# Kernel optimization log

Hardware: AMD Instinct MI355X
Metric: run time of the kernel (lower is better)

Reference implementation:

```python
import jax, jax.numpy as jnp
import numpy as np

B, T, D = 2, 2048, 2048
N_HEADS, N_KV, HEAD_DIM = 16, 8, 128
SOFTCAP = 50.0
BIG_NEG = -2.3819763e38
ROPE_BASE = 10000.0


def apply_rope(x, positions):
    # x: [B, L, N, H], positions: [B, L]
    H = x.shape[-1]
    half = H // 2
    fraction = 2.0 * jnp.arange(half, dtype=jnp.float32) / H
    timescale = ROPE_BASE ** fraction  # [H/2]
    sinusoid = positions.astype(jnp.float32)[:, :, None, None] / timescale[None, None, None, :]  # [B,L,1,H/2]
    sin, cos = jnp.sin(sinusoid), jnp.cos(sinusoid)
    first, second = jnp.split(x, 2, axis=-1)
    out = jnp.concatenate([first * cos - second * sin, second * cos + first * sin], axis=-1)
    return out.astype(x.dtype)


def setup_inputs() -> dict:
    key = jax.random.key(0)
    k1, k2, k3, k4 = jax.random.split(key, 4)
    x = jax.random.normal(k1, (B, T, D), dtype=jnp.float32)
    positions = jnp.broadcast_to(jnp.arange(T, dtype=jnp.int32), (B, T))
    # causal mask [B, 1, T, S]
    attn_mask = jnp.broadcast_to(jnp.tril(jnp.ones((T, T), dtype=bool))[None, None], (B, 1, T, T))
    s = 1.0 / np.sqrt(D)
    w_q = jax.random.normal(k2, (N_HEADS, D, HEAD_DIM), dtype=jnp.float32) * s
    w_kv = jax.random.normal(k3, (2, N_KV, D, HEAD_DIM), dtype=jnp.float32) * s
    w_out = jax.random.normal(k4, (N_HEADS, HEAD_DIM, D), dtype=jnp.float32) * (1.0 / np.sqrt(N_HEADS * HEAD_DIM))
    return {"x": x, "positions": positions, "attn_mask": attn_mask, "w_q": w_q, "w_kv": w_kv, "w_out": w_out}


def reference(x, positions, attn_mask, w_q, w_kv, w_out):
    # projections (GQA branch: num_kv_heads != num_heads)
    q = jnp.einsum('btd,ndh->btnh', x, w_q)            # [B,T,N,H]
    kv = jnp.einsum('bsd,cndh->cbsnh', x, w_kv)        # [2,B,S,K,H]
    k, v = kv[0], kv[1]
    q = apply_rope(q, positions) * (HEAD_DIM ** -0.5)  # rsqrt_head_dim
    k = apply_rope(k, positions)
    G = N_HEADS // N_KV
    q = q.reshape(B, T, N_KV, G, HEAD_DIM)             # B T K G H
    logits = jnp.einsum('btkgh,bskh->bkgts', q, k).astype(jnp.float32)
    logits = jnp.tanh(logits / SOFTCAP) * SOFTCAP
    masked = jnp.where(attn_mask[:, :, None, :, :], logits, BIG_NEG)
    probs = jax.nn.softmax(masked, axis=-1).astype(k.dtype)
    encoded = jnp.einsum('bkgts,bskh->btkgh', probs, v).reshape(B, T, N_HEADS, HEAD_DIM)
    return jnp.einsum('btnh,nhd->btd', encoded, w_out)
```

## Files before the change

### kernel.cpp

```cpp
#include <hip/hip_runtime.h>


typedef unsigned short u16;
typedef __attribute__((ext_vector_type(8))) short short8;
typedef __attribute__((ext_vector_type(4))) float floatx4;

static __device__ __forceinline__ u16 f2b(float f){
  unsigned u = __float_as_uint(f);
  u = (u + 0x7fffu + ((u >> 16) & 1u)) >> 16;
  return (u16)u;
}
static __device__ __forceinline__ float b2f(u16 u){
  return __uint_as_float(((unsigned)u) << 16);
}
static __device__ __forceinline__ void gload16(const u16* g, u16* l){
  __builtin_amdgcn_global_load_lds(
      (const __attribute__((address_space(1))) unsigned int*)g,
      (__attribute__((address_space(3))) unsigned int*)l, 16, 0, 0);
}

static __device__ void tr64(const float* __restrict__ s, u16* __restrict__ d,
                            int sRS, int dRS, float (*t)[65], int tid){
  #pragma unroll
  for(int i = 0; i < 16; i++){
    int idx = tid + 256 * i;
    t[idx >> 6][idx & 63] = s[(long)(idx >> 6) * sRS + (idx & 63)];
  }
  __syncthreads();
  #pragma unroll
  for(int i = 0; i < 16; i++){
    int idx = tid + 256 * i;
    d[(long)(idx >> 6) * dRS + (idx & 63)] = f2b(t[idx & 63][idx >> 6]);
  }
}

__global__ __launch_bounds__(256) void k_prep(
    const float* __restrict__ x, u16* __restrict__ xb,
    const float* __restrict__ wq, u16* __restrict__ wq_t,
    const float* __restrict__ wkv, u16* __restrict__ wkv_t,
    const float* __restrict__ wo, u16* __restrict__ wo_t,
    const int* __restrict__ pos, float* __restrict__ tab){
  __shared__ float t[64][65];
  int blk = blockIdx.x, tid = threadIdx.x;
  if(blk < 8192){
    int i = blk * 256 + tid;
    float4 v = ((const float4*)x)[i];
    ushort4 o = make_ushort4(f2b(v.x), f2b(v.y), f2b(v.z), f2b(v.w));
    ((ushort4*)xb)[i] = o;
  } else if(blk < 9216){
    int q = blk - 8192;
    int bx = q & 1, by = (q >> 1) & 31, bz = q >> 6;
    tr64(wq + (long)bz * 262144 + (long)by * 64 * 128 + bx * 64,
         wq_t + (long)bz * 262144 + (long)bx * 64 * 2048 + by * 64, 128, 2048, t, tid);
  } else if(blk < 10240){
    int q = blk - 9216;
    int bx = q & 1, by = (q >> 1) & 31, bz = q >> 6;
    tr64(wkv + (long)bz * 262144 + (long)by * 64 * 128 + bx * 64,
         wkv_t + (long)bz * 262144 + (long)bx * 64 * 2048 + by * 64, 128, 2048, t, tid);
  } else if(blk < 11264){
    int q = blk - 10240;
    int bx = q & 31, by = q >> 5;
    tr64(wo + (long)by * 64 * 2048 + bx * 64,
         wo_t + (long)bx * 64 * 2048 + by * 64, 2048, 2048, t, tid);
  } else {
    int idx = (blk - 11264) * 256 + tid;
    int row = idx >> 6, h = idx & 63;
    float pf = (float)pos[row];
    float inv = exp2f(-0.20762050593045077f * (float)h);
    float ang = pf * inv;
    tab[(row << 7) + h]      = sinf(ang);
    tab[(row << 7) + 64 + h] = cosf(ang);
  }
}

#define STAGE_A(tt, h) do{ \
  const u16* s_ = Ag + (tt) * 64 + (h) * 262144; \
  u16* d_ = ld + ss * 8192; \
  gload16(s_, d_); gload16(s_ + 131072, d_ + 4096); \
  ss++; if(ss == 10) ss = 0; }while(0)
#define STAGE_B(tt, h) do{ \
  const u16* s_ = Bg + (tt) * 64 + (h) * 262144; \
  u16* d_ = ld + ss * 8192; \
  gload16(s_, d_); gload16(s_ + 131072, d_ + 4096); \
  ss++; if(ss == 10) ss = 0; }while(0)

__global__ __launch_bounds__(512, 2) void k_gemm_qkv(
    const u16* __restrict__ A, const u16* __restrict__ wq_t, const u16* __restrict__ wkv_t,
    const float* __restrict__ tab,
    u16* __restrict__ qb, u16* __restrict__ kb, u16* __restrict__ vtp){
  __shared__ __attribute__((aligned(16))) u16 ring[81920];
  int lin = blockIdx.x + (blockIdx.y << 4);
  int xcd = lin & 7, jj = lin >> 3;
  int mt = (xcd & 3) * 4 + (jj & 3);
  int nt = (xcd >> 2) * 8 + (jj >> 2);
  const u16* Bt = (nt < 8) ? (wq_t + (long)nt * 524288)
                           : (wkv_t + (long)(nt - 8) * 524288);
  int tid = threadIdx.x;
  int lane = tid & 63, wave = tid >> 6, l15 = lane & 15, quad = lane >> 4;
  int wr = wave >> 2, wc = wave & 3;
  int cq0 = quad ^ (l15 & 7), cq1 = cq0 ^ 4;
  int srow = tid >> 3;
  int gch  = (tid & 7) ^ (srow & 7);
  const u16* Ag = A  + ((long)mt * 256 + srow) * 2048 + (gch << 3);
  const u16* Bg = Bt + (long)srow * 2048 + (gch << 3);
  u16* ld = ring + tid * 8;
  int aB = l15 << 6;
  int bB = ((wc & 1) * 64 + l15) << 6;
  int sa = wr;
  int sb = 2 + (wc >> 1);
  int ss = 0;
  floatx4 acc[8][4];
  const floatx4 fz = {0.f, 0.f, 0.f, 0.f};
  #pragma unroll
  for(int m = 0; m < 8; m++)
    #pragma unroll
    for(int n = 0; n < 4; n++) acc[m][n] = fz;

  STAGE_A(0, 0); STAGE_A(0, 1); STAGE_B(0, 0); STAGE_B(0, 1);
  STAGE_A(1, 0); STAGE_A(1, 1);
  asm volatile("s_waitcnt vmcnt(4)" ::: "memory");
  __builtin_amdgcn_s_barrier();

  #pragma unroll 1
  for(int t = 0; t < 32; t++){
    const u16* aS = ring + sa * 8192;
    const u16* bS = ring + sb * 8192;
    int tB = (t < 31) ? t + 1 : 31;
    int tA = (t < 30) ? t + 2 : 31;
    short8 am0k0[4], am0k1[4], am1k0[4], am1k1[4], b0[2], b1[2];
    #pragma unroll
    for(int n = 0; n < 2; n++){
      b0[n] = *(const short8*)(bS + bB + (n << 10) + (cq0 << 3));
      b1[n] = *(const short8*)(bS + bB + (n << 10) + (cq1 << 3));
    }
    #pragma unroll
    for(int m = 0; m < 4; m++){
      am0k0[m] = *(const short8*)(aS + aB + (m << 10) + (cq0 << 3));
      am0k1[m] = *(const short8*)(aS + aB + (m << 10) + (cq1 << 3));
    }
    STAGE_B(tB, 0); STAGE_B(tB, 1);
    __builtin_amdgcn_s_setprio(1);
    #pragma unroll
    for(int m = 0; m < 4; m++)
      #pragma unroll
      for(int n = 0; n < 2; n++)
        acc[m][n] = __builtin_amdgcn_mfma_f32_16x16x32_bf16(am0k0[m], b0[n], acc[m][n], 0, 0, 0);
    #pragma unroll
    for(int m = 0; m < 4; m++)
      #pragma unroll
      for(int n = 0; n < 2; n++)
        acc[m][n] = __builtin_amdgcn_mfma_f32_16x16x32_bf16(am0k1[m], b1[n], acc[m][n], 0, 0, 0);
    __builtin_amdgcn_s_setprio(0);
    #pragma unroll
    for(int m = 0; m < 4; m++){
      am1k0[m] = *(const short8*)(aS + aB + 4096 + (m << 10) + (cq0 << 3));
      am1k1[m] = *(const short8*)(aS + aB + 4096 + (m << 10) + (cq1 << 3));
    }
    STAGE_A(tA, 0);
    __builtin_amdgcn_s_setprio(1);
    #pragma unroll
    for(int m = 0; m < 4; m++)
      #pragma unroll
      for(int n = 0; n < 2; n++)
        acc[4 + m][n] = __builtin_amdgcn_mfma_f32_16x16x32_bf16(am1k0[m], b0[n], acc[4 + m][n], 0, 0, 0);
    #pragma unroll
    for(int m = 0; m < 4; m++)
      #pragma unroll
      for(int n = 0; n < 2; n++)
        acc[4 + m][n] = __builtin_amdgcn_mfma_f32_16x16x32_bf16(am1k1[m], b1[n], acc[4 + m][n], 0, 0, 0);
    __builtin_amdgcn_s_setprio(0);
    #pragma unroll
    for(int n = 0; n < 2; n++){
      b0[n] = *(const short8*)(bS + bB + ((2 + n) << 10) + (cq0 << 3));
      b1[n] = *(const short8*)(bS + bB + ((2 + n) << 10) + (cq1 << 3));
    }
    STAGE_A(tA, 1);
    __builtin_amdgcn_s_setprio(1);
    #pragma unroll
    for(int m = 0; m < 4; m++)
      #pragma unroll
      for(int n = 0; n < 2; n++)
        acc[4 + m][2 + n] = __builtin_amdgcn_mfma_f32_16x16x32_bf16(am1k0[m], b0[n], acc[4 + m][2 + n], 0, 0, 0);
    #pragma unroll
    for(int m = 0; m < 4; m++)
      #pragma unroll
      for(int n = 0; n < 2; n++)
        acc[4 + m][2 + n] = __builtin_amdgcn_mfma_f32_16x16x32_bf16(am1k1[m], b1[n], acc[4 + m][2 + n], 0, 0, 0);
    #pragma unroll
    for(int m = 0; m < 4; m++)
      #pragma unroll
      for(int n = 0; n < 2; n++)
        acc[m][2 + n] = __builtin_amdgcn_mfma_f32_16x16x32_bf16(am0k0[m], b0[n], acc[m][2 + n], 0, 0, 0);
    #pragma unroll
    for(int m = 0; m < 4; m++)
      #pragma unroll
      for(int n = 0; n < 2; n++)
        acc[m][2 + n] = __builtin_amdgcn_mfma_f32_16x16x32_bf16(am0k1[m], b1[n], acc[m][2 + n], 0, 0, 0);
    __builtin_amdgcn_s_setprio(0);
    asm volatile("s_waitcnt vmcnt(4)" ::: "memory");
    __builtin_amdgcn_s_barrier();
    sa += 4; if(sa >= 10) sa -= 10;
    sb += 4; if(sb >= 10) sb -= 10;
  }

  asm volatile("s_waitcnt vmcnt(0)" ::: "memory");
  __syncthreads();
  u16* sT = ring;
  int grow0 = mt * 256;
  int hb = wc >> 1, wcl = wc & 1;
  #pragma unroll 1
  for(int hh = 0; hh < 2; hh++){
    if(hb == hh){
      #pragma unroll
      for(int m = 0; m < 8; m++){
        int row = wr * 128 + m * 16 + quad * 4;
        #pragma unroll
        for(int n = 0; n < 4; n++){
          int colh = wcl * 64 + n * 16 + l15;
          #pragma unroll
          for(int j = 0; j < 4; j++)
            sT[(row + j) * 132 + colh] = f2b(acc[m][n][j]);
        }
      }
    }
    __syncthreads();
    if(nt < 12){
      float scale = (nt < 8) ? 0.08838834764831845f : 1.0f;
      u16* dst = (nt < 8) ? qb : kb;
      int dS   = (nt < 8) ? 2048 : 1024;
      int dcol = (nt < 8) ? (nt * 2 + hh) * 128 : ((nt - 8) * 2 + hh) * 128;
      #pragma unroll
      for(int it = 0; it < 16; it++){
        int idx = tid + 512 * it;
        int row = idx >> 5, cw = idx & 31;
        int grow = grow0 + row;
        unsigned lo = *(const unsigned*)&sT[row * 132 + 2 * cw];
        unsigned hi = *(const unsigned*)&sT[row * 132 + 64 + 2 * cw];
        float2 sn = *(const float2*)&tab[(grow << 7) + 2 * cw];
        float2 cs = *(const float2*)&tab[(grow << 7) + 64 + 2 * cw];
        float x1a = b2f((u16)lo), x1b = b2f((u16)(lo >> 16));
        float x2a = b2f((u16)hi), x2b = b2f((u16)(hi >> 16));
        float o1a = (x1a * cs.x - x2a * sn.x) * scale;
        float o1b = (x1b * cs.y - x2b * sn.y) * scale;
        float o2a = (x2a * cs.x + x1a * sn.x) * scale;
        float o2b = (x2b * cs.y + x1b * sn.y) * scale;
        unsigned w1 = (unsigned)f2b(o1a) | ((unsigned)f2b(o1b) << 16);
        unsigned w2 = (unsigned)f2b(o2a) | ((unsigned)f2b(o2b) << 16);
        *(unsigned*)&dst[(long)grow * dS + dcol + 2 * cw] = w1;
        *(unsigned*)&dst[(long)grow * dS + dcol + 64 + 2 * cw] = w2;
      }
    } else {
      int b = mt >> 3, kvh = (nt - 12) * 2 + hh;
      u16* vt = vtp + (long)(b * 8 + kvh) * 262144;
      int tcol0 = (mt & 7) * 256;
      int h = tid >> 2, s0 = (tid & 3) * 64;
      #pragma unroll
      for(int i = 0; i < 16; i++){
        int s = s0 + i * 4;
        ushort4 v4 = make_ushort4(sT[(s    ) * 132 + h], sT[(s + 1) * 132 + h],
                                  sT[(s + 2) * 132 + h], sT[(s + 3) * 132 + h]);
        *(ushort4*)&vt[(long)h * 2048 + tcol0 + s] = v4;
      }
    }
    __syncthreads();
  }
}
#undef STAGE_A
#undef STAGE_B

__global__ __launch_bounds__(256) void k_gemm_out(
    const u16* __restrict__ A, const u16* __restrict__ Bt0, float* __restrict__ C){
  __shared__ __attribute__((aligned(16))) u16 sA[128 * 64];
  __shared__ __attribute__((aligned(16))) u16 sB[128 * 64];
  int mt = blockIdx.x, nt = blockIdx.y;
  const u16* Bt = Bt0 + (long)nt * 262144;
  int tid = threadIdx.x;
  int lane = tid & 63, wave = tid >> 6, l15 = lane & 15, quad = lane >> 4;
  int ro = (wave & 1) * 64, co = (wave >> 1) * 64;
  int xm7 = l15 & 7;
  int srow = tid >> 3;
  int gch  = (tid & 7) ^ (srow & 7);
  const u16* Ag = A  + ((long)(mt * 128) + srow) * 2048 + (gch << 3);
  const u16* Bg = Bt + (long)srow * 2048 + (gch << 3);
  u16* lA = sA + tid * 8;
  u16* lB = sB + tid * 8;
  floatx4 acc[4][4];
  const floatx4 fz = {0.f, 0.f, 0.f, 0.f};
  #pragma unroll
  for(int r = 0; r < 4; r++)
    #pragma unroll
    for(int c = 0; c < 4; c++) acc[r][c] = fz;
  for(int k0 = 0; k0 < 2048; k0 += 64){
    #pragma unroll
    for(int r = 0; r < 4; r++){
      gload16(Ag + (long)r * 65536 + k0, lA + r * 2048);
      gload16(Bg + (long)r * 65536 + k0, lB + r * 2048);
    }
    __syncthreads();
    #pragma unroll
    for(int ks = 0; ks < 2; ks++){
      short8 af[4], bfr[4];
      #pragma unroll
      for(int r = 0; r < 4; r++)
        af[r]  = *(const short8*)(sA + ((ro + r * 16 + l15) << 6) + ((((ks << 2) | quad) ^ xm7) << 3));
      #pragma unroll
      for(int c = 0; c < 4; c++)
        bfr[c] = *(const short8*)(sB + ((co + c * 16 + l15) << 6) + ((((ks << 2) | quad) ^ xm7) << 3));
      #pragma unroll
      for(int r = 0; r < 4; r++)
        #pragma unroll
        for(int c = 0; c < 4; c++)
          acc[r][c] = __builtin_amdgcn_mfma_f32_16x16x32_bf16(af[r], bfr[c], acc[r][c], 0, 0, 0);
    }
    __syncthreads();
  }
  long rb0 = (long)mt * 128 + ro + quad * 4;
  #pragma unroll
  for(int r = 0; r < 4; r++)
    #pragma unroll
    for(int c = 0; c < 4; c++){
      int col = nt * 128 + co + c * 16 + l15;
      #pragma unroll
      for(int j = 0; j < 4; j++)
        C[(rb0 + r * 16 + j) * 2048 + col] = acc[r][c][j];
    }
}

__global__ __launch_bounds__(256) void k_flash(
    const u16* __restrict__ qb, const u16* __restrict__ kb,
    const u16* __restrict__ vt, u16* __restrict__ enc){
  __shared__ __attribute__((aligned(16))) u16 sK[2 * 64 * 128];
  __shared__ __attribute__((aligned(16))) u16 sVt[2 * 128 * 64];
  __shared__ __attribute__((aligned(16))) u16 sP[4][16][72];
  int qt = 31 - blockIdx.y;
  int hidx = blockIdx.x;
  int b = hidx >> 4, kv = (hidx >> 1) & 7, g = hidx & 1;
  int tid = threadIdx.x;
  int lane = tid & 63, wave = tid >> 6, l15 = lane & 15, quad = lane >> 4;

  short8 qf[4];
  {
    const u16* qg = qb + ((long)b * 2048 + qt * 64 + wave * 16 + l15) * 2048
                       + (kv * 2 + g) * 128 + quad * 8;
    #pragma unroll
    for(int ks = 0; ks < 4; ks++) qf[ks] = *(const short8*)(qg + ks * 32);
  }

  int krow = tid >> 4;
  int kch  = (tid & 15) ^ krow;
  const u16* Kg = kb + ((long)b * 2048 + krow) * 1024 + kv * 128 + (kch << 3);
  int vrow = tid >> 3;
  int vch  = (tid & 7) ^ (vrow & 7);
  const u16* Vg = vt + ((long)(b * 8 + kv) * 128 + vrow) * 2048 + (vch << 3);
  u16* lK = sK  + tid * 8;
  u16* lV = sVt + tid * 8;
  #pragma unroll
  for(int r = 0; r < 4; r++){
    gload16(Kg + (long)r * 16384, lK + r * 2048);
    gload16(Vg + (long)r * 65536, lV + r * 2048);
  }

  float l_loc[4] = {0.f, 0.f, 0.f, 0.f};
  floatx4 o_acc[8];
  const floatx4 fz = {0.f, 0.f, 0.f, 0.f};
  #pragma unroll
  for(int c = 0; c < 8; c++) o_acc[c] = fz;

  const float c1 = 0.057707801635558536f;
  const float c2 = -144.26950408889634f;
  const float c3 = 72.13475204444817f;

  for(int kt = 0; kt <= qt; kt++){
    int buf = (kt & 1) * 8192;
    __syncthreads();
    if(kt < qt){
      int nb = buf ^ 8192;
      #pragma unroll
      for(int r = 0; r < 4; r++){
        gload16(Kg + (long)(kt + 1) * 65536 + (long)r * 16384, lK + nb + r * 2048);
        gload16(Vg + (kt + 1) * 64 + (long)r * 65536, lV + nb + r * 2048);
      }
    }
    floatx4 s_acc[4];
    #pragma unroll
    for(int c = 0; c < 4; c++) s_acc[c] = fz;
    #pragma unroll
    for(int ks = 0; ks < 4; ks++){
      #pragma unroll
      for(int cb = 0; cb < 4; cb++){
        short8 bk = *(const short8*)(sK + buf + ((cb * 16 + l15) << 7)
                                     + ((((ks << 2) | quad) ^ l15) << 3));
        s_acc[cb] = __builtin_amdgcn_mfma_f32_16x16x32_bf16(qf[ks], bk, s_acc[cb], 0, 0, 0);
      }
    }
    if(kt < qt){
      #pragma unroll
      for(int r = 0; r < 4; r++){
        #pragma unroll
        for(int cb = 0; cb < 4; cb++){
          float s = s_acc[cb][r];
          float u = __builtin_amdgcn_exp2f(c1 * s);
          float d = __builtin_amdgcn_rcpf(u + 1.f);
          float p = __builtin_amdgcn_exp2f(__builtin_fmaf(c2, d, c3));
          l_loc[r] += p;
          sP[wave][quad * 4 + r][cb * 16 + l15] = f2b(p);
        }
      }
    } else {
      int rloc = wave * 16 + quad * 4;
      #pragma unroll
      for(int r = 0; r < 4; r++){
        #pragma unroll
        for(int cb = 0; cb < 4; cb++){
          float s = s_acc[cb][r];
          float u = __builtin_amdgcn_exp2f(c1 * s);
          float d = __builtin_amdgcn_rcpf(u + 1.f);
          float p = __builtin_amdgcn_exp2f(__builtin_fmaf(c2, d, c3));
          if(cb * 16 + l15 > rloc + r) p = 0.f;
          l_loc[r] += p;
          sP[wave][quad * 4 + r][cb * 16 + l15] = f2b(p);
        }
      }
    }
    #pragma unroll
    for(int ks2 = 0; ks2 < 2; ks2++){
      short8 ap = *(const short8*)&sP[wave][l15][ks2 * 32 + quad * 8];
      #pragma unroll
      for(int c = 0; c < 8; c++){
        short8 bv = *(const short8*)(sVt + buf + ((c * 16 + l15) << 6)
                                     + ((((ks2 << 2) | quad) ^ (l15 & 7)) << 3));
        o_acc[c] = __builtin_amdgcn_mfma_f32_16x16x32_bf16(ap, bv, o_acc[c], 0, 0, 0);
      }
    }
  }
  #pragma unroll
  for(int r = 0; r < 4; r++){
    float l = l_loc[r];
    #pragma unroll
    for(int off = 1; off < 16; off <<= 1) l += __shfl_xor(l, off);
    float invl = 1.f / l;
    long rowe = (long)b * 2048 + qt * 64 + wave * 16 + quad * 4 + r;
    #pragma unroll
    for(int c = 0; c < 8; c++)
      enc[rowe * 2048 + (kv * 2 + g) * 128 + c * 16 + l15] = f2b(o_acc[c][r] * invl);
  }
}

extern "C" void kernel_launch(void* const* d_in, const int* in_sizes, int n_in,
                              void* d_out, int out_size, void* d_ws, size_t ws_size,
                              hipStream_t stream){
  const float* x     = (const float*)d_in[0];
  const int*   posi  = (const int*)  d_in[1];
  const float* w_q   = (const float*)d_in[3];
  const float* w_kv  = (const float*)d_in[4];
  const float* w_out = (const float*)d_in[5];
  float* out = (float*)d_out;

  char* w = (char*)d_ws;
  u16* xb     = (u16*)(w);
  u16* wq_t   = (u16*)(w + 16777216);
  u16* wkv_t  = (u16*)(w + 25165824);
  u16* wout_t = (u16*)(w + 33554432);
  u16* q_buf  = (u16*)(w + 41943040);
  u16* k_buf  = (u16*)(w + 58720256);
  u16* v_t    = (u16*)(w + 67108864);
  float* tab  = (float*)(w + 75497472);
  u16* enc    = xb;

  k_prep    <<<12288, 256, 0, stream>>>(x, xb, w_q, wq_t, w_kv, wkv_t, w_out, wout_t, posi, tab);
  k_gemm_qkv<<<dim3(16, 16), 512, 0, stream>>>(xb, wq_t, wkv_t, tab, q_buf, k_buf, v_t);
  k_flash   <<<dim3(32, 32), 256, 0, stream>>>(q_buf, k_buf, v_t, enc);
  k_gemm_out<<<dim3(32, 16), 256, 0, stream>>>(enc, wout_t, out);
}
```

Measured before the change: 311.9 us.

## Double flash query tile to 128 rows with 8 waves sharing K/V loads

The flash kernel now processes 128 query rows per block with 512 threads (8 waves) instead of 64 rows with 256 threads, so each K/V tile loaded into shared memory is reused by twice as many waves. The pipeline is restructured: K is double-buffered while V uses a single buffer loaded per iteration, with explicit vmcnt waits and raw barriers splitting the QK and PV phases. Waves whose rows lie entirely before the current key tile skip work. This halves global K/V traffic but adds more barriers per iteration, and causal imbalance across waves within a block may leave some waves idle.

Measured after the change: 318.1 us. No clear change (+2.0%).

```diff
diff --git a/kernel.cpp b/kernel.cpp
--- a/kernel.cpp
+++ b/kernel.cpp
@@ -326,13 +326,13 @@
     }
 }
 
-__global__ __launch_bounds__(256) void k_flash(
+__global__ __launch_bounds__(512, 4) void k_flash(
     const u16* __restrict__ qb, const u16* __restrict__ kb,
     const u16* __restrict__ vt, u16* __restrict__ enc){
   __shared__ __attribute__((aligned(16))) u16 sK[2 * 64 * 128];
-  __shared__ __attribute__((aligned(16))) u16 sVt[2 * 128 * 64];
-  __shared__ __attribute__((aligned(16))) u16 sP[4][16][72];
-  int qt = 31 - blockIdx.y;
+  __shared__ __attribute__((aligned(16))) u16 sV[128 * 64];
+  __shared__ __attribute__((aligned(16))) u16 sP[8][16][72];
+  int qt = 15 - blockIdx.y;
   int hidx = blockIdx.x;
   int b = hidx >> 4, kv = (hidx >> 1) & 7, g = hidx & 1;
   int tid = threadIdx.x;
@@ -340,25 +340,23 @@
 
   short8 qf[4];
   {
-    const u16* qg = qb + ((long)b * 2048 + qt * 64 + wave * 16 + l15) * 2048
+    const u16* qg = qb + ((long)b * 2048 + qt * 128 + wave * 16 + l15) * 2048
                        + (kv * 2 + g) * 128 + quad * 8;
     #pragma unroll
     for(int ks = 0; ks < 4; ks++) qf[ks] = *(const short8*)(qg + ks * 32);
   }
 
   int krow = tid >> 4;
-  int kch  = (tid & 15) ^ krow;
+  int kch  = (tid & 15) ^ (krow & 15);
   const u16* Kg = kb + ((long)b * 2048 + krow) * 1024 + kv * 128 + (kch << 3);
   int vrow = tid >> 3;
   int vch  = (tid & 7) ^ (vrow & 7);
   const u16* Vg = vt + ((long)(b * 8 + kv) * 128 + vrow) * 2048 + (vch << 3);
-  u16* lK = sK  + tid * 8;
-  u16* lV = sVt + tid * 8;
-  #pragma unroll
-  for(int r = 0; r < 4; r++){
-    gload16(Kg + (long)r * 16384, lK + r * 2048);
-    gload16(Vg + (long)r * 65536, lV + r * 2048);
-  }
+  u16* lK = sK + tid * 8;
+  u16* lV = sV + tid * 8;
+
+  int KT = 2 * qt + 2;
+  gload16(Kg, lK); gload16(Kg + 32768, lK + 4096);
 
   float l_loc[4] = {0.f, 0.f, 0.f, 0.f};
   floatx4 o_acc[8];
@@ -370,68 +368,76 @@
   const float c2 = -144.26950408889634f;
   const float c3 = 72.13475204444817f;
 
-  for(int kt = 0; kt <= qt; kt++){
+  #pragma unroll 1
+  for(int kt = 0; kt < KT; kt++){
     int buf = (kt & 1) * 8192;
-    __syncthreads();
-    if(kt < qt){
-      int nb = buf ^ 8192;
-      #pragma unroll
-      for(int r = 0; r < 4; r++){
-        gload16(Kg + (long)(kt + 1) * 65536 + (long)r * 16384, lK + nb + r * 2048);
-        gload16(Vg + (kt + 1) * 64 + (long)r * 65536, lV + nb + r * 2048);
-      }
-    }
-    floatx4 s_acc[4];
-    #pragma unroll
-    for(int c = 0; c < 4; c++) s_acc[c] = fz;
-    #pragma unroll
-    for(int ks = 0; ks < 4; ks++){
-      #pragma unroll
-      for(int cb = 0; cb < 4; cb++){
-        short8 bk = *(const short8*)(sK + buf + ((cb * 16 + l15) << 7)
-                                     + ((((ks << 2) | quad) ^ l15) << 3));
-        s_acc[cb] = __builtin_amdgcn_mfma_f32_16x16x32_bf16(qf[ks], bk, s_acc[cb], 0, 0, 0);
-      }
-    }
-    if(kt < qt){
-      #pragma unroll
-      for(int r = 0; r < 4; r++){
+    int tn = (kt + 1 < KT) ? kt + 1 : KT - 1;
+    gload16(Vg + kt * 64, lV);
+    gload16(Vg + kt * 64 + 131072, lV + 4096);
+    gload16(Kg + (long)tn * 65536, lK + (buf ^ 8192));
+    gload16(Kg + (long)tn * 65536 + 32768, lK + (buf ^ 8192) + 4096);
+    asm volatile("s_waitcnt vmcnt(4)" ::: "memory");
+    __builtin_amdgcn_s_barrier();
+    int rrel = qt * 128 + wave * 16 - kt * 64;
+    bool act = (rrel + 15 >= 0);
+    if(act){
+      floatx4 s_acc[4];
+      #pragma unroll
+      for(int c = 0; c < 4; c++) s_acc[c] = fz;
+      #pragma unroll
+      for(int ks = 0; ks < 4; ks++){
         #pragma unroll
         for(int cb = 0; cb < 4; cb++){
-          float s = s_acc[cb][r];
-          float u = __builtin_amdgcn_exp2f(c1 * s);
-          float d = __builtin_amdgcn_rcpf(u + 1.f);
-          float p = __builtin_amdgcn_exp2f(__builtin_fmaf(c2, d, c3));
-          l_loc[r] += p;
-          sP[wave][quad * 4 + r][cb * 16 + l15] = f2b(p);
+          short8 bk = *(const short8*)(sK + buf + ((cb * 16 + l15) << 7)
+                                       + ((((ks << 2) | quad) ^ l15) << 3));
+          s_acc[cb] = __builtin_amdgcn_mfma_f32_16x16x32_bf16(qf[ks], bk, s_acc[cb], 0, 0, 0);
         }
       }
-    } else {
-      int rloc = wave * 16 + quad * 4;
-      #pragma unroll
-      for(int r = 0; r < 4; r++){
-        #pragma unroll
-        for(int cb = 0; cb < 4; cb++){
-          float s = s_acc[cb][r];
-          float u = __builtin_amdgcn_exp2f(c1 * s);
-          float d = __builtin_amdgcn_rcpf(u + 1.f);
-          float p = __builtin_amdgcn_exp2f(__builtin_fmaf(c2, d, c3));
-          if(cb * 16 + l15 > rloc + r) p = 0.f;
-          l_loc[r] += p;
-          sP[wave][quad * 4 + r][cb * 16 + l15] = f2b(p);
+      if(rrel >= 63){
+        #pragma unroll
+        for(int r = 0; r < 4; r++){
+          #pragma unroll
+          for(int cb = 0; cb < 4; cb++){
+            float s = s_acc[cb][r];
+            float u = __builtin_amdgcn_exp2f(c1 * s);
+            float d = __builtin_amdgcn_rcpf(u + 1.f);
+            float p = __builtin_amdgcn_exp2f(__builtin_fmaf(c2, d, c3));
+            l_loc[r] += p;
+            sP[wave][quad * 4 + r][cb * 16 + l15] = f2b(p);
+          }
         }
-      }
-    }
-    #pragma unroll
-    for(int ks2 = 0; ks2 < 2; ks2++){
-      short8 ap = *(const short8*)&sP[wave][l15][ks2 * 32 + quad * 8];
-      #pragma unroll
-      for(int c = 0; c < 8; c++){
-        short8 bv = *(const short8*)(sVt + buf + ((c * 16 + l15) << 6)
-                                     + ((((ks2 << 2) | quad) ^ (l15 & 7)) << 3));
-        o_acc[c] = __builtin_amdgcn_mfma_f32_16x16x32_bf16(ap, bv, o_acc[c], 0, 0, 0);
-      }
-    }
+      } else {
+        int dbase = rrel + quad * 4;
+        #pragma unroll
+        for(int r = 0; r < 4; r++){
+          #pragma unroll
+          for(int cb = 0; cb < 4; cb++){
+            float s = s_acc[cb][r];
+            float u = __builtin_amdgcn_exp2f(c1 * s);
+            float d = __builtin_amdgcn_rcpf(u + 1.f);
+            float p = __builtin_amdgcn_exp2f(__builtin_fmaf(c2, d, c3));
+            if(cb * 16 + l15 > dbase + r) p = 0.f;
+            l_loc[r] += p;
+            sP[wave][quad * 4 + r][cb * 16 + l15] = f2b(p);
+          }
+        }
+      }
+    }
+    asm volatile("s_waitcnt vmcnt(2)" ::: "memory");
+    __builtin_amdgcn_s_barrier();
+    if(act){
+      #pragma unroll
+      for(int ks2 = 0; ks2 < 2; ks2++){
+        short8 ap = *(const short8*)&sP[wave][l15][ks2 * 32 + quad * 8];
+        #pragma unroll
+        for(int c = 0; c < 8; c++){
+          short8 bv = *(const short8*)(sV + ((c * 16 + l15) << 6)
+                                       + ((((ks2 << 2) | quad) ^ (l15 & 7)) << 3));
+          o_acc[c] = __builtin_amdgcn_mfma_f32_16x16x32_bf16(ap, bv, o_acc[c], 0, 0, 0);
+        }
+      }
+    }
+    __builtin_amdgcn_s_barrier();
   }
   #pragma unroll
   for(int r = 0; r < 4; r++){
@@ -439,7 +445,7 @@
     #pragma unroll
     for(int off = 1; off < 16; off <<= 1) l += __shfl_xor(l, off);
     float invl = 1.f / l;
-    long rowe = (long)b * 2048 + qt * 64 + wave * 16 + quad * 4 + r;
+    long rowe = (long)b * 2048 + qt * 128 + wave * 16 + quad * 4 + r;
     #pragma unroll
     for(int c = 0; c < 8; c++)
       enc[rowe * 2048 + (kv * 2 + g) * 128 + c * 16 + l15] = f2b(o_acc[c][r] * invl);
@@ -469,6 +475,6 @@
 
   k_prep    <<<12288, 256, 0, stream>>>(x, xb, w_q, wq_t, w_kv, wkv_t, w_out, wout_t, posi, tab);
   k_gemm_qkv<<<dim3(16, 16), 512, 0, stream>>>(xb, wq_t, wkv_t, tab, q_buf, k_buf, v_t);
-  k_flash   <<<dim3(32, 32), 256, 0, stream>>>(q_buf, k_buf, v_t, enc);
+  k_flash   <<<dim3(32, 16), 512, 0, stream>>>(q_buf, k_buf, v_t, enc);
   k_gemm_out<<<dim3(32, 16), 256, 0, stream>>>(enc, wout_t, out);
 }
```

## Process both GQA query heads per block to share K/V tile loads

Applied to the files above, without the earlier changes.

Each flash-attention block now handles both query heads of a KV group, so every K and V tile staged in LDS is used by two sets of MFMAs. This halves the grid and the global K/V traffic. The q-tile order is also changed to mix long and short causal rows. The cost is doubled accumulator registers (two o_acc sets and two score sets), which may lower occupancy, and half as many blocks to spread across CUs.

Result: slower. 356.1 us (+14.2%).

```diff
diff --git a/kernel.cpp b/kernel.cpp
--- a/kernel.cpp
+++ b/kernel.cpp
@@ -332,18 +332,22 @@
   __shared__ __attribute__((aligned(16))) u16 sK[2 * 64 * 128];
   __shared__ __attribute__((aligned(16))) u16 sVt[2 * 128 * 64];
   __shared__ __attribute__((aligned(16))) u16 sP[4][16][72];
-  int qt = 31 - blockIdx.y;
+  int by = blockIdx.y;
+  int qt = (by < 16) ? (31 - by) : (by - 16);
   int hidx = blockIdx.x;
-  int b = hidx >> 4, kv = (hidx >> 1) & 7, g = hidx & 1;
+  int b = hidx >> 3, kv = hidx & 7;
   int tid = threadIdx.x;
   int lane = tid & 63, wave = tid >> 6, l15 = lane & 15, quad = lane >> 4;
 
-  short8 qf[4];
+  short8 qf0[4], qf1[4];
   {
     const u16* qg = qb + ((long)b * 2048 + qt * 64 + wave * 16 + l15) * 2048
-                       + (kv * 2 + g) * 128 + quad * 8;
-    #pragma unroll
-    for(int ks = 0; ks < 4; ks++) qf[ks] = *(const short8*)(qg + ks * 32);
+                       + kv * 256 + quad * 8;
+    #pragma unroll
+    for(int ks = 0; ks < 4; ks++){
+      qf0[ks] = *(const short8*)(qg + ks * 32);
+      qf1[ks] = *(const short8*)(qg + 128 + ks * 32);
+    }
   }
 
   int krow = tid >> 4;
@@ -360,11 +364,12 @@
     gload16(Vg + (long)r * 65536, lV + r * 2048);
   }
 
-  float l_loc[4] = {0.f, 0.f, 0.f, 0.f};
-  floatx4 o_acc[8];
+  float l0[4] = {0.f, 0.f, 0.f, 0.f};
+  float l1[4] = {0.f, 0.f, 0.f, 0.f};
+  floatx4 o0[8], o1[8];
   const floatx4 fz = {0.f, 0.f, 0.f, 0.f};
   #pragma unroll
-  for(int c = 0; c < 8; c++) o_acc[c] = fz;
+  for(int c = 0; c < 8; c++){ o0[c] = fz; o1[c] = fz; }
 
   const float c1 = 0.057707801635558536f;
   const float c2 = -144.26950408889634f;
@@ -381,45 +386,32 @@
         gload16(Vg + (kt + 1) * 64 + (long)r * 65536, lV + nb + r * 2048);
       }
     }
-    floatx4 s_acc[4];
-    #pragma unroll
-    for(int c = 0; c < 4; c++) s_acc[c] = fz;
+    floatx4 s0[4], s1[4];
+    #pragma unroll
+    for(int c = 0; c < 4; c++){ s0[c] = fz; s1[c] = fz; }
     #pragma unroll
     for(int ks = 0; ks < 4; ks++){
       #pragma unroll
       for(int cb = 0; cb < 4; cb++){
         short8 bk = *(const short8*)(sK + buf + ((cb * 16 + l15) << 7)
                                      + ((((ks << 2) | quad) ^ l15) << 3));
-        s_acc[cb] = __builtin_amdgcn_mfma_f32_16x16x32_bf16(qf[ks], bk, s_acc[cb], 0, 0, 0);
-      }
-    }
-    if(kt < qt){
-      #pragma unroll
-      for(int r = 0; r < 4; r++){
-        #pragma unroll
-        for(int cb = 0; cb < 4; cb++){
-          float s = s_acc[cb][r];
-          float u = __builtin_amdgcn_exp2f(c1 * s);
-          float d = __builtin_amdgcn_rcpf(u + 1.f);
-          float p = __builtin_amdgcn_exp2f(__builtin_fmaf(c2, d, c3));
-          l_loc[r] += p;
-          sP[wave][quad * 4 + r][cb * 16 + l15] = f2b(p);
-        }
-      }
-    } else {
-      int rloc = wave * 16 + quad * 4;
-      #pragma unroll
-      for(int r = 0; r < 4; r++){
-        #pragma unroll
-        for(int cb = 0; cb < 4; cb++){
-          float s = s_acc[cb][r];
-          float u = __builtin_amdgcn_exp2f(c1 * s);
-          float d = __builtin_amdgcn_rcpf(u + 1.f);
-          float p = __builtin_amdgcn_exp2f(__builtin_fmaf(c2, d, c3));
-          if(cb * 16 + l15 > rloc + r) p = 0.f;
-          l_loc[r] += p;
-          sP[wave][quad * 4 + r][cb * 16 + l15] = f2b(p);
-        }
+        s0[cb] = __builtin_amdgcn_mfma_f32_16x16x32_bf16(qf0[ks], bk, s0[cb], 0, 0, 0);
+        s1[cb] = __builtin_amdgcn_mfma_f32_16x16x32_bf16(qf1[ks], bk, s1[cb], 0, 0, 0);
+      }
+    }
+    int rloc = wave * 16 + quad * 4;
+    bool diag = (kt == qt);
+    #pragma unroll
+    for(int r = 0; r < 4; r++){
+      #pragma unroll
+      for(int cb = 0; cb < 4; cb++){
+        float s = s0[cb][r];
+        float u = __builtin_amdgcn_exp2f(c1 * s);
+        float d = __builtin_amdgcn_rcpf(u + 1.f);
+        float p = __builtin_amdgcn_exp2f(__builtin_fmaf(c2, d, c3));
+        if(diag && (cb * 16 + l15 > rloc + r)) p = 0.f;
+        l0[r] += p;
+        sP[wave][quad * 4 + r][cb * 16 + l15] = f2b(p);
       }
     }
     #pragma unroll
@@ -429,20 +421,48 @@
       for(int c = 0; c < 8; c++){
         short8 bv = *(const short8*)(sVt + buf + ((c * 16 + l15) << 6)
                                      + ((((ks2 << 2) | quad) ^ (l15 & 7)) << 3));
-        o_acc[c] = __builtin_amdgcn_mfma_f32_16x16x32_bf16(ap, bv, o_acc[c], 0, 0, 0);
+        o0[c] = __builtin_amdgcn_mfma_f32_16x16x32_bf16(ap, bv, o0[c], 0, 0, 0);
+      }
+    }
+    #pragma unroll
+    for(int r = 0; r < 4; r++){
+      #pragma unroll
+      for(int cb = 0; cb < 4; cb++){
+        float s = s1[cb][r];
+        float u = __builtin_amdgcn_exp2f(c1 * s);
+        float d = __builtin_amdgcn_rcpf(u + 1.f);
+        float p = __builtin_amdgcn_exp2f(__builtin_fmaf(c2, d, c3));
+        if(diag && (cb * 16 + l15 > rloc + r)) p = 0.f;
+        l1[r] += p;
+        sP[wave][quad * 4 + r][cb * 16 + l15] = f2b(p);
+      }
+    }
+    #pragma unroll
+    for(int ks2 = 0; ks2 < 2; ks2++){
+      short8 ap = *(const short8*)&sP[wave][l15][ks2 * 32 + quad * 8];
+      #pragma unroll
+      for(int c = 0; c < 8; c++){
+        short8 bv = *(const short8*)(sVt + buf + ((c * 16 + l15) << 6)
+                                     + ((((ks2 << 2) | quad) ^ (l15 & 7)) << 3));
+        o1[c] = __builtin_amdgcn_mfma_f32_16x16x32_bf16(ap, bv, o1[c], 0, 0, 0);
       }
     }
   }
   #pragma unroll
   for(int r = 0; r < 4; r++){
-    float l = l_loc[r];
-    #pragma unroll
-    for(int off = 1; off < 16; off <<= 1) l += __shfl_xor(l, off);
-    float invl = 1.f / l;
+    float la = l0[r], lb = l1[r];
+    #pragma unroll
+    for(int off = 1; off < 16; off <<= 1){
+      la += __shfl_xor(la, off);
+      lb += __shfl_xor(lb, off);
+    }
+    float ia = 1.f / la, ib = 1.f / lb;
     long rowe = (long)b * 2048 + qt * 64 + wave * 16 + quad * 4 + r;
     #pragma unroll
-    for(int c = 0; c < 8; c++)
-      enc[rowe * 2048 + (kv * 2 + g) * 128 + c * 16 + l15] = f2b(o_acc[c][r] * invl);
+    for(int c = 0; c < 8; c++){
+      enc[rowe * 2048 + kv * 256 + c * 16 + l15]       = f2b(o0[c][r] * ia);
+      enc[rowe * 2048 + kv * 256 + 128 + c * 16 + l15] = f2b(o1[c][r] * ib);
+    }
   }
 }
 
@@ -469,6 +489,6 @@
 
   k_prep    <<<12288, 256, 0, stream>>>(x, xb, w_q, wq_t, w_kv, wkv_t, w_out, wout_t, posi, tab);
   k_gemm_qkv<<<dim3(16, 16), 512, 0, stream>>>(xb, wq_t, wkv_t, tab, q_buf, k_buf, v_t);
-  k_flash   <<<dim3(32, 32), 256, 0, stream>>>(q_buf, k_buf, v_t, enc);
+  k_flash   <<<dim3(16, 32), 256, 0, stream>>>(q_buf, k_buf, v_t, enc);
   k_gemm_out<<<dim3(32, 16), 256, 0, stream>>>(enc, wout_t, out);
 }
```
